# Kernel tuning notes

Hardware: AMD Instinct MI355X
Metric: run time of the kernel (lower is better)

## Reference

```python
import jax, jax.numpy as jnp
import numpy as np

N_NODES = 50000
N_EDGES = 800000
IN_FEAT = 256
OUT_FEAT = 256
NUM_RELS = 8
NUM_BASES = 4


def setup_inputs() -> dict:
    key = jax.random.key(0)
    ks = jax.random.split(key, 8)
    feat = jax.random.normal(ks[0], (N_NODES, IN_FEAT), dtype=jnp.float32)
    norm = jax.random.uniform(ks[1], (N_EDGES, 1), dtype=jnp.float32)
    src = jax.random.randint(ks[2], (N_EDGES,), 0, N_NODES)
    dst = jax.random.randint(ks[3], (N_EDGES,), 0, N_NODES)
    etypes = jax.random.randint(ks[4], (N_EDGES,), 0, NUM_RELS)
    # learned parameters (xavier-ish scale)
    weight = jax.random.normal(ks[5], (NUM_BASES, IN_FEAT, OUT_FEAT), dtype=jnp.float32) * (2.0 / np.sqrt(IN_FEAT + OUT_FEAT))
    w_comp = jax.random.normal(ks[6], (NUM_RELS, NUM_BASES), dtype=jnp.float32) * (2.0 / np.sqrt(NUM_RELS + NUM_BASES))
    loop_weight = jax.random.normal(ks[7], (IN_FEAT, OUT_FEAT), dtype=jnp.float32) * (2.0 / np.sqrt(IN_FEAT + OUT_FEAT))
    h_bias = jnp.zeros((OUT_FEAT,), dtype=jnp.float32)
    return {"feat": feat, "weight": weight, "w_comp": w_comp,
            "loop_weight": loop_weight, "h_bias": h_bias,
            "norm": norm, "src": src, "dst": dst, "etypes": etypes}


def reference(feat, weight, w_comp, loop_weight, h_bias, norm, src, dst, etypes):
    # basis decomposition: W_r = sum_b a_{rb} V_b  -> [R, in, out]
    W = jnp.einsum('rb,bio->rio', w_comp, weight)
    # relation-grouped GEMM: transform every node by every relation. [N, R, out]
    Hr = jnp.einsum('ni,rio->nro', feat, W)
    # per-edge message: gather (src node, edge relation) then apply edge norm. [E, out]
    msg = Hr[src, etypes] * norm
    # scatter-reduce (sum) messages to destination nodes. [N, out]
    agg = jax.ops.segment_sum(msg, dst, num_segments=N_NODES)
    # self-loop + bias + activation (dropout rate 0.0 -> identity)
    out = agg + feat @ loop_weight + h_bias
    return jax.nn.relu(out)
```

## Files before the change

### kernel.cpp

```cpp
#include <hip/hip_runtime.h>
#include <stdint.h>

typedef unsigned short u16;
typedef __bf16 bf16x8 __attribute__((ext_vector_type(8)));
typedef float f32x4 __attribute__((ext_vector_type(4)));

#define N_NODES 50000
#define N_PAD   50048
#define NUM_E   800000
#define FDIM    256
#define NREL    8
#define NBASE   4
#define KBLK    5
#define NKSTEP  20
#define NSEG    N_NODES
#define NBLK    49
#define MTILES  196

#define PREP_FEAT_BLOCKS 12512
#define PREP_WT_BLOCKS   1280
#define PREP_ZERO_BLOCKS 196

__device__ __forceinline__ u16 f2bf(float f) {
  uint32_t u = __float_as_uint(f);
  u += 0x7FFFu + ((u >> 16) & 1u);
  return (u16)(u >> 16);
}
__device__ __forceinline__ float bf2f(u16 h) {
  return __uint_as_float(((uint32_t)h) << 16);
}

__device__ __forceinline__ void gload_lds16(const void* g, void* l) {
  __builtin_amdgcn_global_load_lds(
      (__attribute__((address_space(1))) uint32_t*)(void*)(uintptr_t)g,
      (__attribute__((address_space(3))) uint32_t*)(uintptr_t)l,
      16, 0, 0);
}

__global__ __launch_bounds__(256) void prep_k(const float* __restrict__ feat,
                                              const float* __restrict__ weight,
                                              const float* __restrict__ loop_w,
                                              u16* __restrict__ fb,
                                              u16* __restrict__ Wb_all,
                                              int* __restrict__ cnt) {
  const int b = blockIdx.x;
  const int tid = threadIdx.x;
  if (b < PREP_FEAT_BLOCKS) {
    int idx = b * 256 + tid;
    int row = idx >> 6;
    int q = (idx & 63) * 4;
    float4 v = make_float4(0.f, 0.f, 0.f, 0.f);
    if (row < N_NODES) v = *reinterpret_cast<const float4*>(feat + (size_t)row * FDIM + q);
    ushort4 h;
    h.x = f2bf(v.x); h.y = f2bf(v.y); h.z = f2bf(v.z); h.w = f2bf(v.w);
    *reinterpret_cast<ushort4*>(fb + (size_t)row * FDIM + q) = h;
  } else if (b < PREP_FEAT_BLOCKS + PREP_WT_BLOCKS) {
    int idx = (b - PREP_FEAT_BLOCKS) * 256 + tid;
    int r = idx >> 16, rem = idx & 65535;
    int o = rem >> 8, i = rem & 255;
    float s = (r < NBASE) ? weight[(size_t)r * 65536 + i * 256 + o]
                          : loop_w[i * 256 + o];
    Wb_all[idx] = f2bf(s);
  } else {
    int i = (b - PREP_FEAT_BLOCKS - PREP_WT_BLOCKS) * 256 + tid;
    if (i < NSEG) cnt[i] = 0;
  }
}

__global__ __launch_bounds__(256) void hist_k(const int* __restrict__ dst,
                                              int* __restrict__ cnt) {
  int e = blockIdx.x * 256 + threadIdx.x;
  if (e < NUM_E) atomicAdd(&cnt[dst[e]], 1);
}

__global__ __launch_bounds__(1024) void scan1(const int* __restrict__ cnt,
                                              int* __restrict__ rowstart,
                                              int* __restrict__ blocksum) {
  __shared__ int wtot[16], woff[16];
  const int tid = threadIdx.x, lane = tid & 63, w = tid >> 6;
  const int i = blockIdx.x * 1024 + tid;
  const int v = (i < NSEG) ? cnt[i] : 0;
  int inc = v;
#pragma unroll
  for (int off = 1; off < 64; off <<= 1) {
    int t = __shfl_up(inc, off);
    if (lane >= off) inc += t;
  }
  if (lane == 63) wtot[w] = inc;
  __syncthreads();
  if (w == 0) {
    int tv = (lane < 16) ? wtot[lane] : 0;
    int tinc = tv;
#pragma unroll
    for (int off = 1; off < 16; off <<= 1) {
      int t = __shfl_up(tinc, off);
      if (lane >= off) tinc += t;
    }
    if (lane < 16) woff[lane] = tinc - tv;
    if (lane == 15) blocksum[blockIdx.x] = tinc;
  }
  __syncthreads();
  if (i < NSEG) rowstart[i] = inc - v + woff[w];
}

__global__ __launch_bounds__(512) void scan2(int* __restrict__ blocksum) {
  __shared__ int s[512];
  const int tid = threadIdx.x;
  const int v = (tid < NBLK) ? blocksum[tid] : 0;
  s[tid] = v;
#pragma unroll
  for (int off = 1; off < 512; off <<= 1) {
    __syncthreads();
    int t = (tid >= off) ? s[tid - off] : 0;
    __syncthreads();
    s[tid] += t;
  }
  if (tid < NBLK) blocksum[tid] = s[tid] - v;
}

__global__ __launch_bounds__(1024) void scan3(int* __restrict__ rowstart,
                                              const int* __restrict__ blockoff,
                                              int* __restrict__ cursor) {
  const int i = blockIdx.x * 1024 + threadIdx.x;
  if (i < NSEG) {
    const int v = rowstart[i] + blockoff[i >> 10];
    rowstart[i] = v;
    cursor[i] = v;
  }
  if (i == NSEG) rowstart[NSEG] = NUM_E;
}

__global__ __launch_bounds__(256) void bucket_k(const int* __restrict__ src,
                                                const int* __restrict__ dst,
                                                const int* __restrict__ et,
                                                const float* __restrict__ norm,
                                                int* __restrict__ cursor,
                                                int2* __restrict__ ekv) {
  int e = blockIdx.x * 256 + threadIdx.x;
  if (e >= NUM_E) return;
  const int pos = atomicAdd(&cursor[dst[e]], 1);
  int2 kv;
  kv.x = src[e] * NREL + et[e];
  kv.y = __float_as_int(norm[e]);
  ekv[pos] = kv;
}

__global__ __launch_bounds__(256) void agg_G(const u16* __restrict__ feat_bf,
                                             const int* __restrict__ rowstart,
                                             const int2* __restrict__ ekv,
                                             const float* __restrict__ w_comp,
                                             u16* __restrict__ G) {
  __shared__ float4 wcs4[NREL];
  if (threadIdx.x < NREL) {
    const float* wr = w_comp + threadIdx.x * NBASE;
    wcs4[threadIdx.x] = make_float4(wr[0], wr[1], wr[2], wr[3]);
  }
  __syncthreads();
  const int n = blockIdx.x * 4 + (threadIdx.x >> 6);
  const int lane = threadIdx.x & 63;
  const int beg = rowstart[n], end = rowstart[n + 1];

  f32x4 a0 = {}, a1 = {}, a2 = {}, a3 = {}, a4 = {}, a5 = {}, a6 = {}, a7 = {};
  const u16* fl = feat_bf + lane * 4;

  for (int base = beg; base < end; base += 64) {
    const int m = min(64, end - base);
    int kvi = 0, nvi = 0;
    if (lane < m) {
      const int2 e = ekv[base + lane];
      kvi = e.x; nvi = e.y;
    }
#pragma unroll
    for (int g = 0; g < 8; ++g) {
      if (g * 8 >= m) break;
      ushort4 h[8];
      int ks[8]; float ns[8];
#pragma unroll
      for (int jj = 0; jj < 8; ++jj) {
        const int j = g * 8 + jj;
        ks[jj] = __builtin_amdgcn_readlane(kvi, j);
        ns[jj] = __uint_as_float((unsigned)__builtin_amdgcn_readlane(nvi, j));
        h[jj] = *reinterpret_cast<const ushort4*>(
            fl + ((size_t)((unsigned)ks[jj] >> 3) << 8));
      }
#pragma unroll
      for (int jj = 0; jj < 8; ++jj) {
        const float nm = ns[jj];
        const float f0 = bf2f(h[jj].x), f1 = bf2f(h[jj].y),
                    f2 = bf2f(h[jj].z), f3 = bf2f(h[jj].w);
        switch (ks[jj] & 7) {
          case 0: a0[0]+=f0*nm; a0[1]+=f1*nm; a0[2]+=f2*nm; a0[3]+=f3*nm; break;
          case 1: a1[0]+=f0*nm; a1[1]+=f1*nm; a1[2]+=f2*nm; a1[3]+=f3*nm; break;
          case 2: a2[0]+=f0*nm; a2[1]+=f1*nm; a2[2]+=f2*nm; a2[3]+=f3*nm; break;
          case 3: a3[0]+=f0*nm; a3[1]+=f1*nm; a3[2]+=f2*nm; a3[3]+=f3*nm; break;
          case 4: a4[0]+=f0*nm; a4[1]+=f1*nm; a4[2]+=f2*nm; a4[3]+=f3*nm; break;
          case 5: a5[0]+=f0*nm; a5[1]+=f1*nm; a5[2]+=f2*nm; a5[3]+=f3*nm; break;
          case 6: a6[0]+=f0*nm; a6[1]+=f1*nm; a6[2]+=f2*nm; a6[3]+=f3*nm; break;
          default: a7[0]+=f0*nm; a7[1]+=f1*nm; a7[2]+=f2*nm; a7[3]+=f3*nm; break;
        }
      }
    }
  }

  f32x4 c0 = {}, c1 = {}, c2 = {}, c3 = {};
#define COMB(AR, R) { const float4 w = wcs4[R];                          \
    c0[0]+=w.x*AR[0]; c0[1]+=w.x*AR[1]; c0[2]+=w.x*AR[2]; c0[3]+=w.x*AR[3]; \
    c1[0]+=w.y*AR[0]; c1[1]+=w.y*AR[1]; c1[2]+=w.y*AR[2]; c1[3]+=w.y*AR[3]; \
    c2[0]+=w.z*AR[0]; c2[1]+=w.z*AR[1]; c2[2]+=w.z*AR[2]; c2[3]+=w.z*AR[3]; \
    c3[0]+=w.w*AR[0]; c3[1]+=w.w*AR[1]; c3[2]+=w.w*AR[2]; c3[3]+=w.w*AR[3]; }
  COMB(a0, 0) COMB(a1, 1) COMB(a2, 2) COMB(a3, 3)
  COMB(a4, 4) COMB(a5, 5) COMB(a6, 6) COMB(a7, 7)
#undef COMB

  const size_t gbase = (size_t)n * (NBASE * FDIM) + lane * 4;
  ushort4 hh;
  hh.x = f2bf(c0[0]); hh.y = f2bf(c0[1]); hh.z = f2bf(c0[2]); hh.w = f2bf(c0[3]);
  *reinterpret_cast<ushort4*>(G + gbase + 0 * FDIM) = hh;
  hh.x = f2bf(c1[0]); hh.y = f2bf(c1[1]); hh.z = f2bf(c1[2]); hh.w = f2bf(c1[3]);
  *reinterpret_cast<ushort4*>(G + gbase + 1 * FDIM) = hh;
  hh.x = f2bf(c2[0]); hh.y = f2bf(c2[1]); hh.z = f2bf(c2[2]); hh.w = f2bf(c2[3]);
  *reinterpret_cast<ushort4*>(G + gbase + 2 * FDIM) = hh;
  hh.x = f2bf(c3[0]); hh.y = f2bf(c3[1]); hh.z = f2bf(c3[2]); hh.w = f2bf(c3[3]);
  *reinterpret_cast<ushort4*>(G + gbase + 3 * FDIM) = hh;
}

__global__ __launch_bounds__(512, 2) void fused_gemm(const u16* __restrict__ G,
                                                     const u16* __restrict__ feat_bf,
                                                     const u16* __restrict__ Wb_all,
                                                     const float* __restrict__ bias,
                                                     float* __restrict__ out) {
  __shared__ __align__(16) u16 As[2][256 * 64];
  __shared__ __align__(16) u16 Bs[2][256 * 64];
  const int tid = threadIdx.x;
  const int lane = tid & 63;
  const int w = tid >> 6;
  const int wm = w >> 2, wn = w & 3;
  const int mtile = blockIdx.x;

  const int srow = tid >> 3;
  const int scolx = ((tid & 7) << 3) ^ ((srow & 7) << 3);

  f32x4 acc[8][4] = {};

  auto stage = [&](int ks, int buf) {
    const int r = ks >> 2, kk4 = ks & 3;
    const int kcol = kk4 * 64 + scolx;
#pragma unroll
    for (int q = 0; q < 4; ++q) {
      const int arow = q * 64 + srow;
      int gr = mtile * 256 + arow;
      if (gr >= N_PAD) gr = N_PAD - 1;
      const u16* asrc = (r < NBASE)
          ? G + (size_t)gr * 1024 + r * 256 + kcol
          : feat_bf + (size_t)gr * 256 + kcol;
      gload_lds16(asrc, &As[buf][q * 4096 + tid * 8]);
      const u16* bsrc = Wb_all + (size_t)r * 65536 + (size_t)arow * 256 + kcol;
      gload_lds16(bsrc, &Bs[buf][q * 4096 + tid * 8]);
    }
  };

  stage(0, 0);
  __syncthreads();
  for (int t = 0; t < NKSTEP; ++t) {
    const int cur = t & 1;
    if (t + 1 < NKSTEP) stage(t + 1, cur ^ 1);
#pragma unroll
    for (int kk = 0; kk < 2; ++kk) {
      const int colx = (kk * 32 + ((lane >> 4) << 3)) ^ ((lane & 7) << 3);
      bf16x8 a[8], b[4];
#pragma unroll
      for (int mf = 0; mf < 8; ++mf)
        a[mf] = *reinterpret_cast<const bf16x8*>(
            &As[cur][(wm * 128 + mf * 16 + (lane & 15)) * 64 + colx]);
#pragma unroll
      for (int nf = 0; nf < 4; ++nf)
        b[nf] = *reinterpret_cast<const bf16x8*>(
            &Bs[cur][(wn * 64 + nf * 16 + (lane & 15)) * 64 + colx]);
      __builtin_amdgcn_s_setprio(1);
#pragma unroll
      for (int mf = 0; mf < 8; ++mf)
#pragma unroll
        for (int nf = 0; nf < 4; ++nf)
          acc[mf][nf] = __builtin_amdgcn_mfma_f32_16x16x32_bf16(b[nf], a[mf], acc[mf][nf], 0, 0, 0);
      __builtin_amdgcn_s_setprio(0);
    }
    __syncthreads();
  }

#pragma unroll
  for (int mf = 0; mf < 8; ++mf) {
    const int m = mtile * 256 + wm * 128 + mf * 16 + (lane & 15);
    if (m >= N_NODES) continue;
#pragma unroll
    for (int nf = 0; nf < 4; ++nf) {
      const int o0 = wn * 64 + nf * 16 + ((lane >> 4) << 2);
      const float4 bv = *reinterpret_cast<const float4*>(bias + o0);
      float4 v;
      v.x = fmaxf(acc[mf][nf][0] + bv.x, 0.f);
      v.y = fmaxf(acc[mf][nf][1] + bv.y, 0.f);
      v.z = fmaxf(acc[mf][nf][2] + bv.z, 0.f);
      v.w = fmaxf(acc[mf][nf][3] + bv.w, 0.f);
      *reinterpret_cast<float4*>(out + (size_t)m * 256 + o0) = v;
    }
  }
}

extern "C" void kernel_launch(void* const* d_in, const int* in_sizes, int n_in,
                              void* d_out, int out_size, void* d_ws, size_t ws_size,
                              hipStream_t stream) {
  (void)in_sizes; (void)n_in; (void)out_size; (void)ws_size;
  const float* feat   = (const float*)d_in[0];
  const float* weight = (const float*)d_in[1];
  const float* w_comp = (const float*)d_in[2];
  const float* loop_w = (const float*)d_in[3];
  const float* h_bias = (const float*)d_in[4];
  const float* norm   = (const float*)d_in[5];
  const int*   src    = (const int*)d_in[6];
  const int*   dst    = (const int*)d_in[7];
  const int*   et     = (const int*)d_in[8];
  float* out = (float*)d_out;

  char* ws = (char*)d_ws;
  u16*   feat_bf  = (u16*)(ws);
  u16*   Wb_all   = (u16*)(ws + 25624576);
  u16*   G        = (u16*)(ws + 26279936);
  int*   counts   = (int*)(ws + 128778240);
  int*   rowstart = (int*)(ws + 128978432);
  int*   cursor   = (int*)(ws + 129178880);
  int2*  ekv      = (int2*)(ws + 129379072);
  int*   blocksum = (int*)(ws + 135779072);

  prep_k<<<PREP_FEAT_BLOCKS + PREP_WT_BLOCKS + PREP_ZERO_BLOCKS, 256, 0, stream>>>(
      feat, weight, loop_w, feat_bf, Wb_all, counts);

  hist_k<<<(NUM_E + 255) / 256, 256, 0, stream>>>(dst, counts);
  scan1<<<NBLK, 1024, 0, stream>>>(counts, rowstart, blocksum);
  scan2<<<1, 512, 0, stream>>>(blocksum);
  scan3<<<NBLK + 1, 1024, 0, stream>>>(rowstart, blocksum, cursor);
  bucket_k<<<(NUM_E + 255) / 256, 256, 0, stream>>>(src, dst, et, norm, cursor, ekv);

  agg_G<<<N_NODES / 4, 256, 0, stream>>>(feat_bf, rowstart, ekv, w_comp, G);

  fused_gemm<<<MTILES, 512, 0, stream>>>(G, feat_bf, Wb_all, h_bias, out);
}
```

Baseline: 229.9 us.

## Bucket edges by (dst, relation) to drop per-edge relation switch in aggregation

Edges are now counting-sorted by the composite key dst*NREL+etype instead of dst alone, so each destination's edges arrive grouped by relation. The aggregation kernel walks each relation segment with a single accumulator and a one-ahead prefetch, then folds it into the basis outputs. This replaces the eight-way switch and eight accumulator sets with a simpler loop and fewer registers. In exchange the histogram, scan and cursor arrays grow eightfold, and the edge loop is now serial with only one load in flight where it used to issue eight gathers together.

```diff
diff --git a/kernel.cpp b/kernel.cpp
--- a/kernel.cpp
+++ b/kernel.cpp
@@ -13,13 +13,13 @@
 #define NBASE   4
 #define KBLK    5
 #define NKSTEP  20
-#define NSEG    N_NODES
-#define NBLK    49
+#define NSEG    (N_NODES * NREL)
+#define NBLK    391
 #define MTILES  196
 
 #define PREP_FEAT_BLOCKS 12512
 #define PREP_WT_BLOCKS   1280
-#define PREP_ZERO_BLOCKS 196
+#define PREP_ZERO_BLOCKS 1563
 
 __device__ __forceinline__ u16 f2bf(float f) {
   uint32_t u = __float_as_uint(f);
@@ -68,9 +68,10 @@
 }
 
 __global__ __launch_bounds__(256) void hist_k(const int* __restrict__ dst,
+                                              const int* __restrict__ et,
                                               int* __restrict__ cnt) {
   int e = blockIdx.x * 256 + threadIdx.x;
-  if (e < NUM_E) atomicAdd(&cnt[dst[e]], 1);
+  if (e < NUM_E) atomicAdd(&cnt[dst[e] * NREL + et[e]], 1);
 }
 
 __global__ __launch_bounds__(1024) void scan1(const int* __restrict__ cnt,
@@ -138,9 +139,9 @@
                                                 int2* __restrict__ ekv) {
   int e = blockIdx.x * 256 + threadIdx.x;
   if (e >= NUM_E) return;
-  const int pos = atomicAdd(&cursor[dst[e]], 1);
+  const int pos = atomicAdd(&cursor[dst[e] * NREL + et[e]], 1);
   int2 kv;
-  kv.x = src[e] * NREL + et[e];
+  kv.x = src[e];
   kv.y = __float_as_int(norm[e]);
   ekv[pos] = kv;
 }
@@ -158,59 +159,48 @@
   __syncthreads();
   const int n = blockIdx.x * 4 + (threadIdx.x >> 6);
   const int lane = threadIdx.x & 63;
-  const int beg = rowstart[n], end = rowstart[n + 1];
-
-  f32x4 a0 = {}, a1 = {}, a2 = {}, a3 = {}, a4 = {}, a5 = {}, a6 = {}, a7 = {};
   const u16* fl = feat_bf + lane * 4;
 
-  for (int base = beg; base < end; base += 64) {
-    const int m = min(64, end - base);
-    int kvi = 0, nvi = 0;
-    if (lane < m) {
-      const int2 e = ekv[base + lane];
-      kvi = e.x; nvi = e.y;
-    }
-#pragma unroll
-    for (int g = 0; g < 8; ++g) {
-      if (g * 8 >= m) break;
-      ushort4 h[8];
-      int ks[8]; float ns[8];
-#pragma unroll
-      for (int jj = 0; jj < 8; ++jj) {
-        const int j = g * 8 + jj;
-        ks[jj] = __builtin_amdgcn_readlane(kvi, j);
-        ns[jj] = __uint_as_float((unsigned)__builtin_amdgcn_readlane(nvi, j));
-        h[jj] = *reinterpret_cast<const ushort4*>(
-            fl + ((size_t)((unsigned)ks[jj] >> 3) << 8));
+  int rs[9];
+#pragma unroll
+  for (int r = 0; r < 9; ++r) rs[r] = rowstart[n * NREL + r];
+
+  f32x4 c0 = {}, c1 = {}, c2 = {}, c3 = {};
+
+#pragma unroll
+  for (int r = 0; r < NREL; ++r) {
+    int p = rs[r];
+    const int e = rs[r + 1];
+    if (p < e) {
+      f32x4 ar = {};
+      int2 ed = ekv[p];
+      float nm0 = __uint_as_float((unsigned)__builtin_amdgcn_readfirstlane(ed.y));
+      int src0 = __builtin_amdgcn_readfirstlane(ed.x);
+      ushort4 h0 = *reinterpret_cast<const ushort4*>(fl + ((size_t)src0 << 8));
+      while (true) {
+        ushort4 h1;
+        float nm1 = 0.f;
+        const bool more = (p + 1 < e);
+        if (more) {
+          const int2 ed1 = ekv[p + 1];
+          nm1 = __uint_as_float((unsigned)__builtin_amdgcn_readfirstlane(ed1.y));
+          const int src1 = __builtin_amdgcn_readfirstlane(ed1.x);
+          h1 = *reinterpret_cast<const ushort4*>(fl + ((size_t)src1 << 8));
+        }
+        ar[0] += bf2f(h0.x) * nm0;
+        ar[1] += bf2f(h0.y) * nm0;
+        ar[2] += bf2f(h0.z) * nm0;
+        ar[3] += bf2f(h0.w) * nm0;
+        if (!more) break;
+        h0 = h1; nm0 = nm1; ++p;
       }
-#pragma unroll
-      for (int jj = 0; jj < 8; ++jj) {
-        const float nm = ns[jj];
-        const float f0 = bf2f(h[jj].x), f1 = bf2f(h[jj].y),
-                    f2 = bf2f(h[jj].z), f3 = bf2f(h[jj].w);
-        switch (ks[jj] & 7) {
-          case 0: a0[0]+=f0*nm; a0[1]+=f1*nm; a0[2]+=f2*nm; a0[3]+=f3*nm; break;
-          case 1: a1[0]+=f0*nm; a1[1]+=f1*nm; a1[2]+=f2*nm; a1[3]+=f3*nm; break;
-          case 2: a2[0]+=f0*nm; a2[1]+=f1*nm; a2[2]+=f2*nm; a2[3]+=f3*nm; break;
-          case 3: a3[0]+=f0*nm; a3[1]+=f1*nm; a3[2]+=f2*nm; a3[3]+=f3*nm; break;
-          case 4: a4[0]+=f0*nm; a4[1]+=f1*nm; a4[2]+=f2*nm; a4[3]+=f3*nm; break;
-          case 5: a5[0]+=f0*nm; a5[1]+=f1*nm; a5[2]+=f2*nm; a5[3]+=f3*nm; break;
-          case 6: a6[0]+=f0*nm; a6[1]+=f1*nm; a6[2]+=f2*nm; a6[3]+=f3*nm; break;
-          default: a7[0]+=f0*nm; a7[1]+=f1*nm; a7[2]+=f2*nm; a7[3]+=f3*nm; break;
-        }
-      }
-    }
-  }
-
-  f32x4 c0 = {}, c1 = {}, c2 = {}, c3 = {};
-#define COMB(AR, R) { const float4 w = wcs4[R];                          \
-    c0[0]+=w.x*AR[0]; c0[1]+=w.x*AR[1]; c0[2]+=w.x*AR[2]; c0[3]+=w.x*AR[3]; \
-    c1[0]+=w.y*AR[0]; c1[1]+=w.y*AR[1]; c1[2]+=w.y*AR[2]; c1[3]+=w.y*AR[3]; \
-    c2[0]+=w.z*AR[0]; c2[1]+=w.z*AR[1]; c2[2]+=w.z*AR[2]; c2[3]+=w.z*AR[3]; \
-    c3[0]+=w.w*AR[0]; c3[1]+=w.w*AR[1]; c3[2]+=w.w*AR[2]; c3[3]+=w.w*AR[3]; }
-  COMB(a0, 0) COMB(a1, 1) COMB(a2, 2) COMB(a3, 3)
-  COMB(a4, 4) COMB(a5, 5) COMB(a6, 6) COMB(a7, 7)
-#undef COMB
+      const float4 w = wcs4[r];
+      c0[0] += w.x * ar[0]; c0[1] += w.x * ar[1]; c0[2] += w.x * ar[2]; c0[3] += w.x * ar[3];
+      c1[0] += w.y * ar[0]; c1[1] += w.y * ar[1]; c1[2] += w.y * ar[2]; c1[3] += w.y * ar[3];
+      c2[0] += w.z * ar[0]; c2[1] += w.z * ar[1]; c2[2] += w.z * ar[2]; c2[3] += w.z * ar[3];
+      c3[0] += w.w * ar[0]; c3[1] += w.w * ar[1]; c3[2] += w.w * ar[2]; c3[3] += w.w * ar[3];
+    }
+  }
 
   const size_t gbase = (size_t)n * (NBASE * FDIM) + lane * 4;
   ushort4 hh;
@@ -325,15 +315,15 @@
   u16*   Wb_all   = (u16*)(ws + 25624576);
   u16*   G        = (u16*)(ws + 26279936);
   int*   counts   = (int*)(ws + 128778240);
-  int*   rowstart = (int*)(ws + 128978432);
-  int*   cursor   = (int*)(ws + 129178880);
-  int2*  ekv      = (int2*)(ws + 129379072);
-  int*   blocksum = (int*)(ws + 135779072);
+  int*   rowstart = (int*)(ws + 130378240);
+  int*   cursor   = (int*)(ws + 131978496);
+  int2*  ekv      = (int2*)(ws + 133578496);
+  int*   blocksum = (int*)(ws + 139978496);
 
   prep_k<<<PREP_FEAT_BLOCKS + PREP_WT_BLOCKS + PREP_ZERO_BLOCKS, 256, 0, stream>>>(
       feat, weight, loop_w, feat_bf, Wb_all, counts);
 
-  hist_k<<<(NUM_E + 255) / 256, 256, 0, stream>>>(dst, counts);
+  hist_k<<<(NUM_E + 255) / 256, 256, 0, stream>>>(dst, et, counts);
   scan1<<<NBLK, 1024, 0, stream>>>(counts, rowstart, blocksum);
   scan2<<<1, 512, 0, stream>>>(blocksum);
   scan3<<<NBLK + 1, 1024, 0, stream>>>(rowstart, blocksum, cursor);
```

Measured after the change: 240.2 us. 4.5% more time.
